# Performance work log

Measured on AMD Instinct MI355X. Metric: run time of the kernel, lower is better.

The kernel has to match this reference:

```python
import jax, jax.numpy as jnp
import numpy as np

D = 8
W = 256
CX = 63   # in_channels_xyz
CD = 27   # in_channels_dir
CF = 3    # in_channels_fea
SKIPS = (4,)
B = 262144


def _linear_init(k, fin, fout):
    # matches torch nn.Linear default: U(-1/sqrt(fin), 1/sqrt(fin))
    k1, k2 = jax.random.split(k)
    s = 1.0 / np.sqrt(fin)
    w = jax.random.uniform(k1, (fin, fout), jnp.float32, -s, s)
    b = jax.random.uniform(k2, (fout,), jnp.float32, -s, s)
    return w, b


def setup_inputs() -> dict:
    key = jax.random.key(0)
    ks = jax.random.split(key, 16)
    inp = {"x": jax.random.normal(ks[0], (B, CX + CD + CF), jnp.float32)}
    for i in range(D):
        fin = CX if i == 0 else (W + CX if i in SKIPS else W)
        w, b = _linear_init(ks[1 + i], fin, W)
        inp[f"w{i}"] = w
        inp[f"b{i}"] = b
    inp["wf"], inp["bf"] = _linear_init(ks[10], W, W)                 # xyz_encoding_final
    inp["wd"], inp["bd"] = _linear_init(ks[11], W + CD + CF, W // 2)  # dir_encoding
    inp["ws"], inp["bs"] = _linear_init(ks[12], W, 1)                 # sigma head
    inp["wr"], inp["br"] = _linear_init(ks[13], W // 2, 3)            # rgb head
    return inp


def reference(x, w0, b0, w1, b1, w2, b2, w3, b3, w4, b4, w5, b5, w6, b6, w7, b7,
              wf, bf, wd, bd, ws, bs, wr, br):
    layers = [(w0, b0), (w1, b1), (w2, b2), (w3, b3),
              (w4, b4), (w5, b5), (w6, b6), (w7, b7)]
    input_xyz = x[:, :CX]            # (B, 63)
    dir_fea = x[:, CX:]              # (B, 30) = dir(27) + feature(3)
    h = input_xyz
    for i, (w, b) in enumerate(layers):
        if i in SKIPS:
            h = jnp.concatenate([input_xyz, h], axis=-1)
        h = jax.nn.relu(h @ w + b)   # (B, 256)
    sigma = h @ ws + bs              # (B, 1)
    xyz_final = h @ wf + bf          # (B, 256), no activation
    d = jax.nn.relu(jnp.concatenate([xyz_final, dir_fea], axis=-1) @ wd + bd)  # (B, 128)
    rgb = jax.nn.sigmoid(d @ wr + br)  # (B, 3)
    return jnp.concatenate([rgb, sigma], axis=-1)  # (B, 4)
```

## Files before the change

### kernel.cpp

```cpp
#include <hip/hip_runtime.h>

typedef __bf16  bf16x8 __attribute__((ext_vector_type(8)));
typedef float   f32x4  __attribute__((ext_vector_type(4)));
typedef unsigned int uint32x2 __attribute__((ext_vector_type(2)));

#define MFMA16(a,b,c) __builtin_amdgcn_mfma_f32_16x16x32_bf16((a),(b),(c),0,0,0)

template<int V> struct ic_t { static constexpr int value = V; };

enum : int {
    OFF_W0 = 0,
    OFF_W1 = OFF_W0 + 256 * 64,
    OFF_W2 = OFF_W1 + 256 * 256,
    OFF_W3 = OFF_W2 + 256 * 256,
    OFF_W4 = OFF_W3 + 256 * 256,
    OFF_W5 = OFF_W4 + 256 * 320,
    OFF_W6 = OFF_W5 + 256 * 256,
    OFF_W7 = OFF_W6 + 256 * 256,
    OFF_WF = OFF_W7 + 256 * 256,
    OFF_WD = OFF_WF + 256 * 256,
    W_TOTAL = OFF_WD + 128 * 288
};

__device__ __forceinline__ unsigned short f2bf(float f) {
    unsigned int u = __float_as_uint(f);
    u += 0x7FFFu + ((u >> 16) & 1u);
    return (unsigned short)(u >> 16);
}

__device__ __forceinline__ void prep_one(const float* __restrict__ src,
                                         unsigned short* __restrict__ dst,
                                         int fout, int Kp, int n1, int n2, int n3,
                                         int idx) {
    int n = idx / Kp;
    int k = idx - n * Kp;
    float v = 0.f;
    if (k < n1)                 v = src[k * fout + n];
    else if (k >= n2 && k < n3) v = src[(k - (n2 - n1)) * fout + n];
    dst[n * Kp + k] = f2bf(v);
}

__global__ void prep_kernel(const float* w0, const float* w1, const float* w2,
                            const float* w3, const float* w4, const float* w5,
                            const float* w6, const float* w7, const float* wf,
                            const float* wd, unsigned short* dst) {
    int i = blockIdx.x * 256 + threadIdx.x;
    if (i < 256 * 64)  { prep_one(w0, dst + OFF_W0, 256,  64,  63,  64,  64, i); return; }
    i -= 256 * 64;
    if (i < 256 * 256) { prep_one(w1, dst + OFF_W1, 256, 256, 256, 256, 256, i); return; }
    i -= 256 * 256;
    if (i < 256 * 256) { prep_one(w2, dst + OFF_W2, 256, 256, 256, 256, 256, i); return; }
    i -= 256 * 256;
    if (i < 256 * 256) { prep_one(w3, dst + OFF_W3, 256, 256, 256, 256, 256, i); return; }
    i -= 256 * 256;
    if (i < 256 * 320) { prep_one(w4, dst + OFF_W4, 256, 320,  63,  64, 320, i); return; }
    i -= 256 * 320;
    if (i < 256 * 256) { prep_one(w5, dst + OFF_W5, 256, 256, 256, 256, 256, i); return; }
    i -= 256 * 256;
    if (i < 256 * 256) { prep_one(w6, dst + OFF_W6, 256, 256, 256, 256, 256, i); return; }
    i -= 256 * 256;
    if (i < 256 * 256) { prep_one(w7, dst + OFF_W7, 256, 256, 256, 256, 256, i); return; }
    i -= 256 * 256;
    if (i < 256 * 256) { prep_one(wf, dst + OFF_WF, 256, 256, 256, 256, 256, i); return; }
    i -= 256 * 256;
    if (i < 128 * 288) { prep_one(wd, dst + OFF_WD, 128, 288, 286, 288, 288, i); return; }
}

struct Params {
    const float* x;
    const unsigned short* Wt;
    const float* b[8];
    const float* bfv;
    const float* bdv;
    const float* wsv;
    const float* bsv;
    const float* wrv;
    const float* brv;
    float* out;
};

__global__ __launch_bounds__(256, 2) void nerf_kernel(Params P) {
    __shared__ char Hs0[32768];
    __shared__ char Hs1[32768];
    __shared__ char Xs[8192];
    __shared__ char Ds[4096];

    const int t    = threadIdx.x;
    const int lane = t & 63;
    const int wave = t >> 6;
    const int lr   = lane & 15;
    const int lk   = lane >> 4;
    const int blockRow = blockIdx.x << 6;

    bf16x8 bp0[4], bp1[4], bp2[4];
    {
        const unsigned short* Wb0 = P.Wt + OFF_W0 + (size_t)((wave << 6) + lr) * 64 + (lk << 3);
#pragma unroll
        for (int nt = 0; nt < 4; ++nt) {
            bp0[nt] = *(const bf16x8*)(Wb0 + (size_t)(nt << 4) * 64);
            bp1[nt] = *(const bf16x8*)(Wb0 + (size_t)(nt << 4) * 64 + 32);
        }
    }

    {
        const float4* xb = (const float4*)(P.x + (size_t)blockRow * 93);
        for (int i = t; i < 1488; i += 256) {
            float4 v = xb[i];
            float vv[4] = {v.x, v.y, v.z, v.w};
#pragma unroll
            for (int j = 0; j < 4; ++j) {
                int e = (i << 2) + j;
                int r = e / 93;
                int c = e - r * 93;
                __bf16 us = (__bf16)vv[j];
                if (c < 63)
                    *(__bf16*)(Xs + ((r * 128 + c * 2) ^ ((r & 7) << 4))) = us;
                else
                    *(__bf16*)(Ds + ((r * 64 + (c - 63) * 2) ^ ((r & 3) << 4))) = us;
            }
        }
        if (t < 64) {
            int r = t;
            *(__bf16*)(Xs + ((r * 128 + 126) ^ ((r & 7) << 4))) = (__bf16)0.f;
            *(__bf16*)(Ds + ((r * 64 + 60) ^ ((r & 3) << 4))) = (__bf16)0.f;
            *(__bf16*)(Ds + ((r * 64 + 62) ^ ((r & 3) << 4))) = (__bf16)0.f;
        }
    }
    __syncthreads();

    auto ldH = [&](const char* B, int mt, int kt) -> bf16x8 {
        int row = (mt << 4) + lr;
        int off = (row * 512 + (kt << 6) + (lk << 4)) ^ ((row & 7) << 4);
        return *(const bf16x8*)(B + off);
    };
    auto ldXs = [&](int mt, int kt) -> bf16x8 {
        int row = (mt << 4) + lr;
        int off = (row * 128 + (kt << 6) + (lk << 4)) ^ ((row & 7) << 4);
        return *(const bf16x8*)(Xs + off);
    };
    auto ldDs = [&](int mt) -> bf16x8 {
        int row = (mt << 4) + lr;
        int off = (row * 64 + (lk << 4)) ^ ((row & 3) << 4);
        return *(const bf16x8*)(Ds + off);
    };

    auto gemm = [&](auto KTt, auto NTt, auto NTnt, auto&& getA,
                    const unsigned short* W, int Kp, const float* bias, bool dorelu,
                    char* dst, const unsigned short* Wn, int Kpn, int cbn) {
        constexpr int KT  = decltype(KTt)::value;
        constexpr int NT  = decltype(NTt)::value;
        constexpr int NTn = decltype(NTnt)::value;
        const int colbase = wave * (NT << 4);
        const unsigned short* Wb = W + (size_t)(colbase + lr) * Kp + (lk << 3);
        const unsigned short* Wbn = (NTn > 0) ? Wn + (size_t)(cbn + lr) * Kpn + (lk << 3) : nullptr;

        f32x4 acc[4][NT];
        {
            f32x4 bfr[NT];
#pragma unroll
            for (int nt = 0; nt < NT; ++nt)
                bfr[nt] = *(const f32x4*)(bias + colbase + (nt << 4) + (lk << 2));
#pragma unroll
            for (int mt = 0; mt < 4; ++mt)
#pragma unroll
                for (int nt = 0; nt < NT; ++nt) acc[mt][nt] = bfr[nt];
        }

        bf16x8 aC[4], aN[4];
#pragma unroll
        for (int mt = 0; mt < 4; ++mt) { aC[mt] = getA(mt, 0); aN[mt] = aC[mt]; }

#pragma unroll
        for (int kt = 0; kt < KT; ++kt) {
            if (kt + 2 < KT) {
#pragma unroll
                for (int nt = 0; nt < NT; ++nt)
                    bp2[nt] = *(const bf16x8*)(Wb + (size_t)(nt << 4) * Kp + ((kt + 2) << 5));
            } else if (NTn > 0) {
#pragma unroll
                for (int nt = 0; nt < (NTn > 0 ? NTn : 1); ++nt)
                    bp2[nt] = *(const bf16x8*)(Wbn + (size_t)(nt << 4) * Kpn + ((kt + 2 - KT) << 5));
            }
            if (kt + 1 < KT) {
#pragma unroll
                for (int mt = 0; mt < 4; ++mt) aN[mt] = getA(mt, kt + 1);
            }
            __builtin_amdgcn_s_setprio(1);
#pragma unroll
            for (int nt = 0; nt < NT; ++nt) {
#pragma unroll
                for (int mt = 0; mt < 4; ++mt)
                    acc[mt][nt] = MFMA16(bp0[nt], aC[mt], acc[mt][nt]);
            }
            __builtin_amdgcn_s_setprio(0);
#pragma unroll
            for (int nt = 0; nt < 4; ++nt) { bp0[nt] = bp1[nt]; bp1[nt] = bp2[nt]; }
#pragma unroll
            for (int mt = 0; mt < 4; ++mt) aC[mt] = aN[mt];
        }

#pragma unroll
        for (int nt = 0; nt < NT; ++nt) {
#pragma unroll
            for (int mt = 0; mt < 4; ++mt) {
                f32x4 v = acc[mt][nt];
                if (dorelu) {
#pragma unroll
                    for (int e = 0; e < 4; ++e) v[e] = fmaxf(v[e], 0.f);
                }
                unsigned int lo, hi;
                asm("v_cvt_pk_bf16_f32 %0, %1, %2" : "=v"(lo) : "v"(v[0]), "v"(v[1]));
                asm("v_cvt_pk_bf16_f32 %0, %1, %2" : "=v"(hi) : "v"(v[2]), "v"(v[3]));
                int batch = (mt << 4) + lr;
                int off = (batch * 512 + ((colbase + (nt << 4) + (lk << 2)) << 1)) ^ ((batch & 7) << 4);
                uint32x2 w2 = {lo, hi};
                *(uint32x2*)(dst + off) = w2;
            }
        }
    };

    const unsigned short* Wt = P.Wt;
    char* cur = Hs0;
    char* alt = Hs1;

    gemm(ic_t<2>{}, ic_t<4>{}, ic_t<4>{},
         [&](int mt, int kt) { return ldXs(mt, kt); },
         Wt + OFF_W0, 64, P.b[0], true, cur, Wt + OFF_W1, 256, wave << 6);
    __syncthreads();

    {
        const unsigned short* Wc[3] = {Wt + OFF_W1, Wt + OFF_W2, Wt + OFF_W3};
        const unsigned short* Wn[3] = {Wt + OFF_W2, Wt + OFF_W3, Wt + OFF_W4};
        const int Kpn[3] = {256, 256, 320};
        const float* bc[3] = {P.b[1], P.b[2], P.b[3]};
        for (int i = 0; i < 3; ++i) {
            gemm(ic_t<8>{}, ic_t<4>{}, ic_t<4>{},
                 [&](int mt, int kt) { return ldH(cur, mt, kt); },
                 Wc[i], 256, bc[i], true, alt, Wn[i], Kpn[i], wave << 6);
            __syncthreads();
            char* tmp = cur; cur = alt; alt = tmp;
        }
    }

    gemm(ic_t<10>{}, ic_t<4>{}, ic_t<4>{},
         [&](int mt, int kt) { return (kt < 2) ? ldXs(mt, kt) : ldH(cur, mt, kt - 2); },
         Wt + OFF_W4, 320, P.b[4], true, alt, Wt + OFF_W5, 256, wave << 6);
    __syncthreads();
    { char* tmp = cur; cur = alt; alt = tmp; }

    {
        const unsigned short* Wc[3] = {Wt + OFF_W5, Wt + OFF_W6, Wt + OFF_W7};
        const unsigned short* Wn[3] = {Wt + OFF_W6, Wt + OFF_W7, Wt + OFF_WF};
        const float* bc[3] = {P.b[5], P.b[6], P.b[7]};
        for (int i = 0; i < 3; ++i) {
            gemm(ic_t<8>{}, ic_t<4>{}, ic_t<4>{},
                 [&](int mt, int kt) { return ldH(cur, mt, kt); },
                 Wc[i], 256, bc[i], true, alt, Wn[i], 256, wave << 6);
            __syncthreads();
            char* tmp = cur; cur = alt; alt = tmp;
        }
    }

    float sig;
    {
        int rr = t >> 2, q = t & 3;
        float sp = 0.f;
#pragma unroll
        for (int j = 0; j < 8; ++j) {
            int cb = (q << 6) + (j << 3);
            bf16x8 h8 = *(const bf16x8*)(cur + ((rr * 512 + (cb << 1)) ^ ((rr & 7) << 4)));
#pragma unroll
            for (int e = 0; e < 8; ++e) sp += (float)h8[e] * P.wsv[cb + e];
        }
        sp += __shfl_xor(sp, 1);
        sp += __shfl_xor(sp, 2);
        sig = sp + P.bsv[0];
    }

    gemm(ic_t<8>{}, ic_t<4>{}, ic_t<2>{},
         [&](int mt, int kt) { return ldH(cur, mt, kt); },
         Wt + OFF_WF, 256, P.bfv, false, alt, Wt + OFF_WD, 288, wave << 5);
    __syncthreads();
    { char* tmp = cur; cur = alt; alt = tmp; }

    gemm(ic_t<9>{}, ic_t<2>{}, ic_t<0>{},
         [&](int mt, int kt) { return (kt < 8) ? ldH(cur, mt, kt) : ldDs(mt); },
         Wt + OFF_WD, 288, P.bdv, true, alt, nullptr, 0, 0);
    __syncthreads();

    {
        int rr = t >> 2, q = t & 3;
        float c0 = 0.f, c1 = 0.f, c2 = 0.f;
#pragma unroll
        for (int j = 0; j < 4; ++j) {
            int kb = (q << 5) + (j << 3);
            bf16x8 d8 = *(const bf16x8*)(alt + ((rr * 512 + (kb << 1)) ^ ((rr & 7) << 4)));
#pragma unroll
            for (int e = 0; e < 8; ++e) {
                float dv = (float)d8[e];
                const float* w = P.wrv + (kb + e) * 3;
                c0 += dv * w[0]; c1 += dv * w[1]; c2 += dv * w[2];
            }
        }
        c0 += __shfl_xor(c0, 1); c0 += __shfl_xor(c0, 2);
        c1 += __shfl_xor(c1, 1); c1 += __shfl_xor(c1, 2);
        c2 += __shfl_xor(c2, 1); c2 += __shfl_xor(c2, 2);
        if (q == 0) {
            float4 o;
            o.x = 1.f / (1.f + __expf(-(c0 + P.brv[0])));
            o.y = 1.f / (1.f + __expf(-(c1 + P.brv[1])));
            o.z = 1.f / (1.f + __expf(-(c2 + P.brv[2])));
            o.w = sig;
            ((float4*)P.out)[blockRow + rr] = o;
        }
    }
}

extern "C" void kernel_launch(void* const* d_in, const int* in_sizes, int n_in,
                              void* d_out, int out_size, void* d_ws, size_t ws_size,
                              hipStream_t stream) {
    const float* x = (const float*)d_in[0];
    const float* w[8];
    const float* b[8];
    for (int i = 0; i < 8; ++i) {
        w[i] = (const float*)d_in[1 + 2 * i];
        b[i] = (const float*)d_in[2 + 2 * i];
    }
    const float* wf  = (const float*)d_in[17];
    const float* bfv = (const float*)d_in[18];
    const float* wd  = (const float*)d_in[19];
    const float* bdv = (const float*)d_in[20];
    const float* wsv = (const float*)d_in[21];
    const float* bsv = (const float*)d_in[22];
    const float* wrv = (const float*)d_in[23];
    const float* brv = (const float*)d_in[24];

    unsigned short* Wt = (unsigned short*)d_ws;

    prep_kernel<<<(W_TOTAL + 255) / 256, 256, 0, stream>>>(
        w[0], w[1], w[2], w[3], w[4], w[5], w[6], w[7], wf, wd, Wt);

    Params P;
    P.x = x; P.Wt = Wt;
    for (int i = 0; i < 8; ++i) P.b[i] = b[i];
    P.bfv = bfv; P.bdv = bdv; P.wsv = wsv; P.bsv = bsv; P.wrv = wrv; P.brv = brv;
    P.out = (float*)d_out;

    nerf_kernel<<<262144 / 64, 256, 0, stream>>>(P);
}
```

Measured before the change: 605.5 us.

## Use single LDS activation buffer and load inputs from global to raise occupancy

Replaces the double-buffered activation tiles and the Xs/Ds input staging with one 32 KB shared buffer. Each GEMM now waits on a barrier before writing its output in place. The xyz and dir/feature inputs are read straight from global memory, with bf16 conversion, inside the A-operand loader. Launch bounds move from 2 to 4 blocks per CU, and the bp2 prefetch array is scoped per iteration to save registers. The goal is higher occupancy to hide latency, at the cost of scalar, uncoalesced global reads of x during layers 0, 4 and dir, an extra barrier inside each GEMM, and possible register spills under the tighter per-thread register limit.

```diff
diff --git a/kernel.cpp b/kernel.cpp
--- a/kernel.cpp
+++ b/kernel.cpp
@@ -28,6 +28,11 @@
     return (unsigned short)(u >> 16);
 }
 
+__device__ __forceinline__ void soft_barrier() {
+    asm volatile("s_waitcnt lgkmcnt(0)" ::: "memory");
+    __builtin_amdgcn_s_barrier();
+}
+
 __device__ __forceinline__ void prep_one(const float* __restrict__ src,
                                          unsigned short* __restrict__ dst,
                                          int fout, int Kp, int n1, int n2, int n3,
@@ -79,11 +84,8 @@
     float* out;
 };
 
-__global__ __launch_bounds__(256, 2) void nerf_kernel(Params P) {
-    __shared__ char Hs0[32768];
-    __shared__ char Hs1[32768];
-    __shared__ char Xs[8192];
-    __shared__ char Ds[4096];
+__global__ __launch_bounds__(256, 4) void nerf_kernel(Params P) {
+    __shared__ char Hs[32768];
 
     const int t    = threadIdx.x;
     const int lane = t & 63;
@@ -92,7 +94,7 @@
     const int lk   = lane >> 4;
     const int blockRow = blockIdx.x << 6;
 
-    bf16x8 bp0[4], bp1[4], bp2[4];
+    bf16x8 bp0[4], bp1[4];
     {
         const unsigned short* Wb0 = P.Wt + OFF_W0 + (size_t)((wave << 6) + lr) * 64 + (lk << 3);
 #pragma unroll
@@ -102,51 +104,25 @@
         }
     }
 
-    {
-        const float4* xb = (const float4*)(P.x + (size_t)blockRow * 93);
-        for (int i = t; i < 1488; i += 256) {
-            float4 v = xb[i];
-            float vv[4] = {v.x, v.y, v.z, v.w};
-#pragma unroll
-            for (int j = 0; j < 4; ++j) {
-                int e = (i << 2) + j;
-                int r = e / 93;
-                int c = e - r * 93;
-                __bf16 us = (__bf16)vv[j];
-                if (c < 63)
-                    *(__bf16*)(Xs + ((r * 128 + c * 2) ^ ((r & 7) << 4))) = us;
-                else
-                    *(__bf16*)(Ds + ((r * 64 + (c - 63) * 2) ^ ((r & 3) << 4))) = us;
-            }
-        }
-        if (t < 64) {
-            int r = t;
-            *(__bf16*)(Xs + ((r * 128 + 126) ^ ((r & 7) << 4))) = (__bf16)0.f;
-            *(__bf16*)(Ds + ((r * 64 + 60) ^ ((r & 3) << 4))) = (__bf16)0.f;
-            *(__bf16*)(Ds + ((r * 64 + 62) ^ ((r & 3) << 4))) = (__bf16)0.f;
-        }
-    }
-    __syncthreads();
-
-    auto ldH = [&](const char* B, int mt, int kt) -> bf16x8 {
+    auto ldXg = [&](int mt, int c0, int lim) -> bf16x8 {
+        const float* xr = P.x + (size_t)(blockRow + (mt << 4) + lr) * 93;
+        bf16x8 r;
+#pragma unroll
+        for (int j = 0; j < 8; ++j) {
+            int c = c0 + (lk << 3) + j;
+            r[j] = (c < lim) ? (__bf16)xr[c] : (__bf16)0.f;
+        }
+        return r;
+    };
+    auto ldH = [&](int mt, int kt) -> bf16x8 {
         int row = (mt << 4) + lr;
         int off = (row * 512 + (kt << 6) + (lk << 4)) ^ ((row & 7) << 4);
-        return *(const bf16x8*)(B + off);
-    };
-    auto ldXs = [&](int mt, int kt) -> bf16x8 {
-        int row = (mt << 4) + lr;
-        int off = (row * 128 + (kt << 6) + (lk << 4)) ^ ((row & 7) << 4);
-        return *(const bf16x8*)(Xs + off);
-    };
-    auto ldDs = [&](int mt) -> bf16x8 {
-        int row = (mt << 4) + lr;
-        int off = (row * 64 + (lk << 4)) ^ ((row & 3) << 4);
-        return *(const bf16x8*)(Ds + off);
+        return *(const bf16x8*)(Hs + off);
     };
 
     auto gemm = [&](auto KTt, auto NTt, auto NTnt, auto&& getA,
                     const unsigned short* W, int Kp, const float* bias, bool dorelu,
-                    char* dst, const unsigned short* Wn, int Kpn, int cbn) {
+                    const unsigned short* Wn, int Kpn, int cbn) {
         constexpr int KT  = decltype(KTt)::value;
         constexpr int NT  = decltype(NTt)::value;
         constexpr int NTn = decltype(NTnt)::value;
@@ -172,6 +148,7 @@
 
 #pragma unroll
         for (int kt = 0; kt < KT; ++kt) {
+            bf16x8 bp2[NT];
             if (kt + 2 < KT) {
 #pragma unroll
                 for (int nt = 0; nt < NT; ++nt)
@@ -180,6 +157,9 @@
 #pragma unroll
                 for (int nt = 0; nt < (NTn > 0 ? NTn : 1); ++nt)
                     bp2[nt] = *(const bf16x8*)(Wbn + (size_t)(nt << 4) * Kpn + ((kt + 2 - KT) << 5));
+            } else {
+#pragma unroll
+                for (int nt = 0; nt < NT; ++nt) bp2[nt] = bp1[nt];
             }
             if (kt + 1 < KT) {
 #pragma unroll
@@ -194,10 +174,14 @@
             }
             __builtin_amdgcn_s_setprio(0);
 #pragma unroll
-            for (int nt = 0; nt < 4; ++nt) { bp0[nt] = bp1[nt]; bp1[nt] = bp2[nt]; }
+            for (int nt = 0; nt < 4; ++nt) { bp0[nt] = bp1[nt]; }
+#pragma unroll
+            for (int nt = 0; nt < NT; ++nt) { bp1[nt] = bp2[nt]; }
 #pragma unroll
             for (int mt = 0; mt < 4; ++mt) aC[mt] = aN[mt];
         }
+
+        soft_barrier();
 
 #pragma unroll
         for (int nt = 0; nt < NT; ++nt) {
@@ -214,19 +198,17 @@
                 int batch = (mt << 4) + lr;
                 int off = (batch * 512 + ((colbase + (nt << 4) + (lk << 2)) << 1)) ^ ((batch & 7) << 4);
                 uint32x2 w2 = {lo, hi};
-                *(uint32x2*)(dst + off) = w2;
+                *(uint32x2*)(Hs + off) = w2;
             }
         }
     };
 
     const unsigned short* Wt = P.Wt;
-    char* cur = Hs0;
-    char* alt = Hs1;
 
     gemm(ic_t<2>{}, ic_t<4>{}, ic_t<4>{},
-         [&](int mt, int kt) { return ldXs(mt, kt); },
-         Wt + OFF_W0, 64, P.b[0], true, cur, Wt + OFF_W1, 256, wave << 6);
-    __syncthreads();
+         [&](int mt, int kt) { return ldXg(mt, kt << 5, 63); },
+         Wt + OFF_W0, 64, P.b[0], true, Wt + OFF_W1, 256, wave << 6);
+    soft_barrier();
 
     {
         const unsigned short* Wc[3] = {Wt + OFF_W1, Wt + OFF_W2, Wt + OFF_W3};
@@ -235,18 +217,16 @@
         const float* bc[3] = {P.b[1], P.b[2], P.b[3]};
         for (int i = 0; i < 3; ++i) {
             gemm(ic_t<8>{}, ic_t<4>{}, ic_t<4>{},
-                 [&](int mt, int kt) { return ldH(cur, mt, kt); },
-                 Wc[i], 256, bc[i], true, alt, Wn[i], Kpn[i], wave << 6);
-            __syncthreads();
-            char* tmp = cur; cur = alt; alt = tmp;
+                 [&](int mt, int kt) { return ldH(mt, kt); },
+                 Wc[i], 256, bc[i], true, Wn[i], Kpn[i], wave << 6);
+            soft_barrier();
         }
     }
 
     gemm(ic_t<10>{}, ic_t<4>{}, ic_t<4>{},
-         [&](int mt, int kt) { return (kt < 2) ? ldXs(mt, kt) : ldH(cur, mt, kt - 2); },
-         Wt + OFF_W4, 320, P.b[4], true, alt, Wt + OFF_W5, 256, wave << 6);
-    __syncthreads();
-    { char* tmp = cur; cur = alt; alt = tmp; }
+         [&](int mt, int kt) { return (kt < 2) ? ldXg(mt, kt << 5, 63) : ldH(mt, kt - 2); },
+         Wt + OFF_W4, 320, P.b[4], true, Wt + OFF_W5, 256, wave << 6);
+    soft_barrier();
 
     {
         const unsigned short* Wc[3] = {Wt + OFF_W5, Wt + OFF_W6, Wt + OFF_W7};
@@ -254,10 +234,9 @@
         const float* bc[3] = {P.b[5], P.b[6], P.b[7]};
         for (int i = 0; i < 3; ++i) {
             gemm(ic_t<8>{}, ic_t<4>{}, ic_t<4>{},
-                 [&](int mt, int kt) { return ldH(cur, mt, kt); },
-                 Wc[i], 256, bc[i], true, alt, Wn[i], 256, wave << 6);
-            __syncthreads();
-            char* tmp = cur; cur = alt; alt = tmp;
+                 [&](int mt, int kt) { return ldH(mt, kt); },
+                 Wc[i], 256, bc[i], true, Wn[i], 256, wave << 6);
+            soft_barrier();
         }
     }
 
@@ -268,7 +247,7 @@
 #pragma unroll
         for (int j = 0; j < 8; ++j) {
             int cb = (q << 6) + (j << 3);
-            bf16x8 h8 = *(const bf16x8*)(cur + ((rr * 512 + (cb << 1)) ^ ((rr & 7) << 4)));
+            bf16x8 h8 = *(const bf16x8*)(Hs + ((rr * 512 + (cb << 1)) ^ ((rr & 7) << 4)));
 #pragma unroll
             for (int e = 0; e < 8; ++e) sp += (float)h8[e] * P.wsv[cb + e];
         }
@@ -278,15 +257,14 @@
     }
 
     gemm(ic_t<8>{}, ic_t<4>{}, ic_t<2>{},
-         [&](int mt, int kt) { return ldH(cur, mt, kt); },
-         Wt + OFF_WF, 256, P.bfv, false, alt, Wt + OFF_WD, 288, wave << 5);
-    __syncthreads();
-    { char* tmp = cur; cur = alt; alt = tmp; }
+         [&](int mt, int kt) { return ldH(mt, kt); },
+         Wt + OFF_WF, 256, P.bfv, false, Wt + OFF_WD, 288, wave << 5);
+    soft_barrier();
 
     gemm(ic_t<9>{}, ic_t<2>{}, ic_t<0>{},
-         [&](int mt, int kt) { return (kt < 8) ? ldH(cur, mt, kt) : ldDs(mt); },
-         Wt + OFF_WD, 288, P.bdv, true, alt, nullptr, 0, 0);
-    __syncthreads();
+         [&](int mt, int kt) { return (kt < 8) ? ldH(mt, kt) : ldXg(mt, 63, 93); },
+         Wt + OFF_WD, 288, P.bdv, true, nullptr, 0, 0);
+    soft_barrier();
 
     {
         int rr = t >> 2, q = t & 3;
@@ -294,7 +272,7 @@
 #pragma unroll
         for (int j = 0; j < 4; ++j) {
             int kb = (q << 5) + (j << 3);
-            bf16x8 d8 = *(const bf16x8*)(alt + ((rr * 512 + (kb << 1)) ^ ((rr & 7) << 4)));
+            bf16x8 d8 = *(const bf16x8*)(Hs + ((rr * 512 + (kb << 1)) ^ ((rr & 7) << 4)));
 #pragma unroll
             for (int e = 0; e < 8; ++e) {
                 float dv = (float)d8[e];
```

Measured after the change: 2.364 ms. 3.9x slower.
